# Kernel tuning notes

Hardware: AMD Instinct MI355X
Metric: run time of the kernel (lower is better)

Reference implementation:

```python
import jax, jax.numpy as jnp
import numpy as np

B, T = 8, 1024          # batch, sequence length
C = 512                 # hidden_channels
FC = 2048               # filter_channels
H = 8                   # n_heads
L = 6                   # n_layers
KS = 3                  # ffn kernel_size
WS = 4                  # relative-attention window_size
KC = C // H             # per-head channels
SCALE = float(KC) ** 0.5
EPS = 1e-5


def setup_inputs():
    key = jax.random.key(0)
    ks = jax.random.split(key, 10)
    def nrm(k, shape, s=0.02):
        return jax.random.normal(k, shape, dtype=jnp.float32) * s
    return {
        "x": jax.random.normal(ks[0], (B, C, T), dtype=jnp.float32),
        "x_mask": jnp.ones((B, 1, T), dtype=jnp.float32),
        "qw": nrm(ks[1], (L, C, C)), "qb": jnp.zeros((L, C), jnp.float32),
        "kw": nrm(ks[2], (L, C, C)), "kb": jnp.zeros((L, C), jnp.float32),
        "vw": nrm(ks[3], (L, C, C)), "vb": jnp.zeros((L, C), jnp.float32),
        "ow": nrm(ks[4], (L, C, C)), "ob": jnp.zeros((L, C), jnp.float32),
        "erk": nrm(ks[5], (L, 2 * WS + 1, KC), KC ** -0.5),
        "erv": nrm(ks[6], (L, 2 * WS + 1, KC), KC ** -0.5),
        "ln1_g": jnp.ones((L, C), jnp.float32), "ln1_b": jnp.zeros((L, C), jnp.float32),
        "fw1": nrm(ks[7], (L, FC, C, KS)), "fb1": jnp.zeros((L, FC), jnp.float32),
        "fw2": nrm(ks[8], (L, C, FC, KS)), "fb2": jnp.zeros((L, C), jnp.float32),
        "ln2_g": jnp.ones((L, C), jnp.float32), "ln2_b": jnp.zeros((L, C), jnp.float32),
    }


def _get_rel_emb(emb, length, ws):
    # emb: [2*ws+1, d] (heads_share=True) -> [2*length-1, d]
    pad = max(length - (ws + 1), 0)
    start = max(ws + 1 - length, 0)
    padded = jnp.pad(emb, ((pad, pad), (0, 0)))
    return padded[start:start + 2 * length - 1]


def _rel_to_abs(x):
    # [b,h,l,2l-1] -> [b,h,l,l]  (VITS pad/reshape trick)
    b, h, l, _ = x.shape
    x = jnp.pad(x, ((0, 0), (0, 0), (0, 0), (0, 1))).reshape(b, h, l * 2 * l)
    x = jnp.pad(x, ((0, 0), (0, 0), (0, l - 1))).reshape(b, h, l + 1, 2 * l - 1)
    return x[:, :, :l, l - 1:]


def _abs_to_rel(x):
    # [b,h,l,l] -> [b,h,l,2l-1]
    b, h, l, _ = x.shape
    x = jnp.pad(x, ((0, 0), (0, 0), (0, 0), (0, l - 1))).reshape(b, h, l * (2 * l - 1))
    x = jnp.pad(x, ((0, 0), (0, 0), (l, 0))).reshape(b, h, l, 2 * l)
    return x[:, :, :, 1:]


def _proj(x, w, b):
    # 1x1 conv1d: x [b,c,t], w [o,c]
    return jnp.einsum('bct,oc->bot', x, w) + b[None, :, None]


def _layer_norm_c(x, g, b):
    # LayerNorm over channel dim of [b,c,t]
    m = jnp.mean(x, axis=1, keepdims=True)
    v = jnp.mean(jnp.square(x - m), axis=1, keepdims=True)
    return (x - m) * jax.lax.rsqrt(v + EPS) * g[None, :, None] + b[None, :, None]


def _attention(x, qw, qb, kw, kb, vw, vb, ow, ob, erk, erv, mask_bias):
    b, _, t = x.shape
    def split_heads(y):
        return y.reshape(b, H, KC, t).transpose(0, 1, 3, 2)  # [b,h,t,kc]
    q = split_heads(_proj(x, qw, qb)) / SCALE
    k = split_heads(_proj(x, kw, kb))
    v = split_heads(_proj(x, vw, vb))
    scores = jnp.einsum('bhtd,bhsd->bhts', q, k)
    rel_k = _get_rel_emb(erk, t, WS)                       # [2t-1, kc]
    scores = scores + _rel_to_abs(jnp.einsum('bhld,md->bhlm', q, rel_k))
    scores = scores + mask_bias
    p = jax.nn.softmax(scores, axis=-1)
    out = jnp.einsum('bhts,bhsd->bhtd', p, v)
    rel_v = _get_rel_emb(erv, t, WS)
    out = out + jnp.einsum('bhlm,md->bhld', _abs_to_rel(p), rel_v)
    out = out.transpose(0, 1, 3, 2).reshape(b, C, t)       # merge heads -> [b,c,t]
    return _proj(out, ow, ob)


def _conv1d(x, w, b):
    pad = ((KS - 1) // 2, KS // 2)  # _same_padding
    y = jax.lax.conv_general_dilated(x, w, (1,), [pad],
                                     dimension_numbers=('NCH', 'OIH', 'NCH'))
    return y + b[None, :, None]


def _ffn(x, x_mask, w1, b1, w2, b2):
    h = jax.nn.relu(_conv1d(x * x_mask, w1, b1))  # activation=None -> relu
    return _conv1d(h * x_mask, w2, b2) * x_mask


def reference(x, x_mask, qw, qb, kw, kb, vw, vb, ow, ob, erk, erv,
              ln1_g, ln1_b, fw1, fb1, fw2, fb2, ln2_g, ln2_b):
    attn_mask = x_mask[:, :, None, :] * x_mask[:, :, :, None]  # [b,1,t,t]
    mask_bias = jnp.where(attn_mask != 0, 0.0, -1e4).astype(x.dtype)
    x = x * x_mask
    for i in range(L):
        y = _attention(x, qw[i], qb[i], kw[i], kb[i], vw[i], vb[i],
                       ow[i], ob[i], erk[i], erv[i], mask_bias)
        x = _layer_norm_c(x + y, ln1_g[i], ln1_b[i])
        y = _ffn(x, x_mask, fw1[i], fb1[i], fw2[i], fb2[i])
        x = _layer_norm_c(x + y, ln2_g[i], ln2_b[i])
    return x * x_mask
```

## Files before the change

### kernel.cpp

```cpp
#include <hip/hip_runtime.h>
#include <hip/hip_bf16.h>
#include <math.h>

#define T_LEN 1024
#define NB    8
#define CCH   512
#define FCH   2048
#define NH    8
#define HD    64
#define NL    6
#define TP    1032
#define LOG2E 1.44269504f

typedef short bf16x8 __attribute__((ext_vector_type(8)));
typedef float f32x4  __attribute__((ext_vector_type(4)));

typedef __attribute__((address_space(1))) const void gvoid_t;
typedef __attribute__((address_space(3))) void lvoid_t;

static __device__ __forceinline__ float b2f(short s) {
    union { unsigned u; float f; } cv; cv.u = ((unsigned)(unsigned short)s) << 16; return cv.f;
}
static __device__ __forceinline__ short f2b(float f) {
    union { __hip_bfloat16 h; short s; } cv; cv.h = __float2bfloat16(f); return cv.s;
}
static __device__ __forceinline__ float exp2_hw(float x) {
    float r; asm("v_exp_f32 %0, %1" : "=v"(r) : "v"(x)); return r;
}

__global__ __launch_bounds__(512)
void conv1_256(const short* __restrict__ Xb, const short* __restrict__ Wb,
               const float* __restrict__ Bias, short* __restrict__ outB)
{
    __shared__ short abuf[2][256 * 64];
    __shared__ short bbuf[2][256 * 64];

    const int tid  = threadIdx.x;
    const int wave = tid >> 6, lane = tid & 63;
    const int l15  = lane & 15, l16 = lane >> 4;
    const int wm   = wave >> 2, wn = wave & 3;
    const int srow = lane >> 3;
    const int xsw  = ((lane & 7) ^ (srow & 7)) << 3;

    const int t0 = blockIdx.x * 256;
    const int o0 = blockIdx.y * 256;
    const int b  = blockIdx.z;

    constexpr int NK = 24;
    const size_t arow0 = (size_t)b * TP + t0;

    auto stageA = [&](int kcg, short* dst) {
        const int tap = kcg >> 3;
        const int c0  = (kcg & 7) << 6;
        const short* base = Xb + (arow0 + tap) * CCH + c0 + xsw;
        #pragma unroll
        for (int i = 0; i < 4; ++i) {
            const int j = wave + 8 * i;
            __builtin_amdgcn_global_load_lds((gvoid_t*)(base + (size_t)(j * 8 + srow) * CCH),
                                             (lvoid_t*)(dst + j * 512), 16, 0, 0);
        }
    };
    auto stageB = [&](int kcg, short* dst) {
        const int tap = kcg >> 3;
        const int c0  = (kcg & 7) << 6;
        const short* base = Wb + ((size_t)tap * FCH + o0) * CCH + c0 + xsw;
        #pragma unroll
        for (int i = 0; i < 4; ++i) {
            const int j = wave + 8 * i;
            __builtin_amdgcn_global_load_lds((gvoid_t*)(base + (size_t)(j * 8 + srow) * CCH),
                                             (lvoid_t*)(dst + j * 512), 16, 0, 0);
        }
    };

    f32x4 acc[8][4];
    #pragma unroll
    for (int i = 0; i < 8; ++i)
        #pragma unroll
        for (int j = 0; j < 4; ++j) acc[i][j] = (f32x4){0.f, 0.f, 0.f, 0.f};

    stageA(0, abuf[0]);
    stageB(0, bbuf[0]);

    for (int kc = 0; kc < NK; ++kc) {
        const int cur = kc & 1, nxt = cur ^ 1;
        const int kn  = (kc + 1 < NK) ? (kc + 1) : kc;

        __builtin_amdgcn_s_barrier();
        stageA(kn, abuf[nxt]);
        asm volatile("s_waitcnt vmcnt(4)" ::: "memory");
        __builtin_amdgcn_s_barrier();

        #pragma unroll
        for (int ks = 0; ks < 2; ++ks) {
            if (ks == 1) stageB(kn, bbuf[nxt]);
            bf16x8 af[8], bfr[4];
            #pragma unroll
            for (int fm = 0; fm < 8; ++fm) {
                const int ra = wm * 128 + fm * 16 + l15;
                af[fm] = *(const bf16x8*)&abuf[cur][ra * 64 + (((ks * 4 + l16) ^ (ra & 7)) << 3)];
            }
            #pragma unroll
            for (int fn = 0; fn < 4; ++fn) {
                const int rb = wn * 64 + fn * 16 + l15;
                bfr[fn] = *(const bf16x8*)&bbuf[cur][rb * 64 + (((ks * 4 + l16) ^ (rb & 7)) << 3)];
            }
            __builtin_amdgcn_s_setprio(1);
            #pragma unroll
            for (int fm = 0; fm < 8; ++fm)
                #pragma unroll
                for (int fn = 0; fn < 4; ++fn)
                    acc[fm][fn] = __builtin_amdgcn_mfma_f32_16x16x32_bf16(
                        af[fm], bfr[fn], acc[fm][fn], 0, 0, 0);
            __builtin_amdgcn_s_setprio(0);
        }
    }

    float bias_v[4];
    #pragma unroll
    for (int fn = 0; fn < 4; ++fn)
        bias_v[fn] = Bias[o0 + wn * 64 + fn * 16 + l15];

    #pragma unroll
    for (int fm = 0; fm < 8; ++fm) {
        #pragma unroll
        for (int r = 0; r < 4; ++r) {
            const int t_loc = wm * 128 + fm * 16 + l16 * 4 + r;
            const size_t orow = (size_t)b * TP + t0 + t_loc + 1;
            #pragma unroll
            for (int fn = 0; fn < 4; ++fn) {
                const int o = o0 + wn * 64 + fn * 16 + l15;
                outB[orow * FCH + o] = f2b(fmaxf(acc[fm][fn][r] + bias_v[fn], 0.f));
            }
        }
    }

    if (t0 == 0)
        for (int cc = tid; cc < 256; cc += 512)
            outB[((size_t)b * TP) * FCH + o0 + cc] = 0;
    if (t0 == T_LEN - 256)
        for (int idx = tid; idx < 7 * 256; idx += 512) {
            const int rr = idx >> 8, cc = idx & 255;
            outB[((size_t)b * TP + 1025 + rr) * FCH + o0 + cc] = 0;
        }
}

template<int KSZ, bool RELU, int OMODE, bool VTOUT>
__global__ __launch_bounds__(256)
void mfma_gemm(const short* __restrict__ Xb, const short* __restrict__ Wb,
               const float* __restrict__ Bias,
               short* __restrict__ outB1, short* __restrict__ outB2,
               short* __restrict__ VTout,
               int Cin, int O, int ksplit)
{
    constexpr int XR = (KSZ == 3) ? 136 : 128;
    __shared__ short shmem[(XR + 128) * 64];
    short* xl = shmem;
    short* wl = shmem + XR * 64;

    const int tid  = threadIdx.x;
    const int wave = tid >> 6, lane = tid & 63;
    const int l15  = lane & 15, l16 = lane >> 4;
    const int wm   = wave >> 1, wn = wave & 1;

    const int t0 = blockIdx.x * 128;
    const int o0 = blockIdx.y * 128;
    const int zz = blockIdx.z;
    const int b     = zz / ksplit;
    const int split = zz - b * ksplit;
    const int kcin  = Cin / ksplit;
    const int cbeg  = split * kcin;

    const size_t xrowbase = (KSZ == 3) ? ((size_t)b * TP + t0) : (size_t)t0;

    const int srow = lane >> 3;
    const int xsw  = ((lane & 7) ^ (srow & 7)) << 3;

    f32x4 acc[4][4];
    #pragma unroll
    for (int i = 0; i < 4; ++i)
        #pragma unroll
        for (int j = 0; j < 4; ++j) acc[i][j] = (f32x4){0.f, 0.f, 0.f, 0.f};

    for (int cb = 0; cb < kcin; cb += 64) {
        const int c0 = cbeg + cb;
        __syncthreads();
        for (int j = wave; j < XR / 8; j += 4) {
            const short* src = Xb + (xrowbase + (size_t)(j * 8 + srow)) * Cin + c0 + xsw;
            __builtin_amdgcn_global_load_lds((gvoid_t*)src, (lvoid_t*)&xl[j * 512], 16, 0, 0);
        }
        #pragma unroll
        for (int kk = 0; kk < KSZ; ++kk) {
            if (kk > 0) __syncthreads();
            for (int j = wave; j < 16; j += 4) {
                const short* src = Wb + ((size_t)kk * O + o0 + j * 8 + srow) * Cin + c0 + xsw;
                __builtin_amdgcn_global_load_lds((gvoid_t*)src, (lvoid_t*)&wl[j * 512], 16, 0, 0);
            }
            __syncthreads();
            #pragma unroll
            for (int ks = 0; ks < 2; ++ks) {
                bf16x8 af[4], bfr[4];
                #pragma unroll
                for (int f = 0; f < 4; ++f) {
                    const int ra = wm * 64 + f * 16 + l15 + (KSZ == 3 ? kk : 0);
                    af[f] = *(const bf16x8*)&xl[ra * 64 + (((ks * 4 + l16) ^ (ra & 7)) << 3)];
                    const int rb = wn * 64 + f * 16 + l15;
                    bfr[f] = *(const bf16x8*)&wl[rb * 64 + (((ks * 4 + l16) ^ (rb & 7)) << 3)];
                }
                #pragma unroll
                for (int fm = 0; fm < 4; ++fm)
                    #pragma unroll
                    for (int fn = 0; fn < 4; ++fn)
                        acc[fm][fn] = __builtin_amdgcn_mfma_f32_16x16x32_bf16(
                            af[fm], bfr[fn], acc[fm][fn], 0, 0, 0);
            }
        }
    }

    float bias_v[4];
    #pragma unroll
    for (int fn = 0; fn < 4; ++fn)
        bias_v[fn] = (OMODE != 2 || split == 0) ? Bias[o0 + wn * 64 + fn * 16 + l15] : 0.f;

    const bool vtblk = VTOUT && (o0 >= 1024);

    if (vtblk) {
        __syncthreads();
        short* tb = shmem;
        #pragma unroll
        for (int fm = 0; fm < 4; ++fm)
            #pragma unroll
            for (int r = 0; r < 4; ++r) {
                const int t_loc = wm * 64 + fm * 16 + l16 * 4 + r;
                #pragma unroll
                for (int fn = 0; fn < 4; ++fn) {
                    const int ol = wn * 64 + fn * 16 + l15;
                    tb[ol * 128 + (((t_loc >> 3) ^ (ol & 7)) << 3) + (t_loc & 7)]
                        = f2b(acc[fm][fn][r] + bias_v[fn]);
                }
            }
        __syncthreads();
        const int bq  = t0 >> 10, tin = t0 & 1023;
        const int vcb = o0 - 1024;
        #pragma unroll
        for (int p = 0; p < 8; ++p) {
            const int drow  = (tid >> 4) + p * 16;
            const int chunk = tid & 15;
            bf16x8 v = *(const bf16x8*)&tb[drow * 128 + ((chunk ^ (drow & 7)) << 3)];
            const int vc = vcb + drow;
            *(bf16x8*)&VTout[((size_t)(bq * NH + (vc >> 6)) * HD + (vc & 63)) * T_LEN
                             + tin + chunk * 8] = v;
        }
    } else {
        #pragma unroll
        for (int fm = 0; fm < 4; ++fm) {
            #pragma unroll
            for (int r = 0; r < 4; ++r) {
                const int t_loc = wm * 64 + fm * 16 + l16 * 4 + r;
                const size_t orow = (KSZ == 3) ? ((size_t)b * T_LEN + t0 + t_loc)
                                               : (size_t)(t0 + t_loc);
                #pragma unroll
                for (int fn = 0; fn < 4; ++fn) {
                    const int o = o0 + wn * 64 + fn * 16 + l15;
                    float v = acc[fm][fn][r] + bias_v[fn];
                    if (RELU) v = fmaxf(v, 0.f);
                    const size_t idx = orow * (size_t)O + o;
                    if (OMODE == 2) {
                        if (split == 0) outB1[idx] = f2b(v);
                        else            outB2[idx] = f2b(v);
                    } else {
                        outB1[idx] = f2b(v);
                    }
                }
            }
        }
    }
}

__global__ __launch_bounds__(512)
void attn_mfma(const short* __restrict__ QKV, const short* __restrict__ VT,
               const float* __restrict__ erk, const float* __restrict__ erv,
               short* __restrict__ Yat)
{
    const int n = blockIdx.x;
    const int c = n & 7, g = n >> 3;
    const int bh = c * 8 + (g & 7);
    const int qt = g >> 3;
    const int b = bh >> 3, h = bh & 7;
    const int tq0 = qt * 128;
    const int hq = h * HD;
    const size_t bt0 = (size_t)b * T_LEN;

    __shared__ short ql[128 * 64];
    __shared__ short pl0[128 * 64];
    __shared__ short kl[2][64 * 64];
    __shared__ short vl[2][64 * 64];
    __shared__ float qerkl[128][12];
    __shared__ float ervl[9][64];

    const int tid  = threadIdx.x;
    const int wave = tid >> 6, lane = tid & 63;
    const int l15  = lane & 15, l16 = lane >> 4;
    const int srow = lane >> 3;
    const int xsw  = ((lane & 7) ^ (srow & 7)) << 3;

    const short* vbase = VT + (size_t)bh * HD * T_LEN;

    for (int j = wave; j < 16; j += 8) {
        const short* src = QKV + (bt0 + tq0 + j * 8 + srow) * 1536 + hq + xsw;
        __builtin_amdgcn_global_load_lds((gvoid_t*)src, (lvoid_t*)&ql[j * 512], 16, 0, 0);
    }
    {
        const short* ksrc = QKV + (bt0 + wave * 8 + srow) * 1536 + 512 + hq + xsw;
        __builtin_amdgcn_global_load_lds((gvoid_t*)ksrc, (lvoid_t*)&kl[0][wave * 512], 16, 0, 0);
        const short* vsrc = vbase + (size_t)(wave * 8 + srow) * T_LEN + xsw;
        __builtin_amdgcn_global_load_lds((gvoid_t*)vsrc, (lvoid_t*)&vl[0][wave * 512], 16, 0, 0);
    }
    for (int i = tid; i < 9 * 64; i += 512) ervl[i >> 6][i & 63] = erv[i];
    __syncthreads();

    bf16x8 af[2];
    #pragma unroll
    for (int ks = 0; ks < 2; ++ks) {
        const int r0 = wave * 16 + l15;
        af[ks] = *(const bf16x8*)&ql[r0 * 64 + (((ks * 4 + l16) ^ (r0 & 7)) << 3)];
    }

    for (int idx = tid; idx < 128 * 9; idx += 512) {
        const int r = idx / 9, o = idx - r * 9;
        float s = 0.f;
        for (int d = 0; d < 64; ++d) {
            float qv = b2f(ql[r * 64 + (((d >> 3) ^ (r & 7)) << 3) + (d & 7)]);
            s += qv * erk[o * 64 + d];
        }
        qerkl[r][o] = s;
    }

    float lsum[4] = {0.f, 0.f, 0.f, 0.f};
    f32x4 acco[4];
    #pragma unroll
    for (int fn = 0; fn < 4; ++fn) acco[fn] = (f32x4){0.f, 0.f, 0.f, 0.f};
    bf16x8 vf[2][4];

    const int ra = wave * 16 + l15;

    for (int it = 0; it < 16; ++it) {
        const int cur = it & 1;
        const int s0  = it * 64;
        __syncthreads();

        if (it < 15) {
            const short* ksrc = QKV + (bt0 + s0 + 64 + wave * 8 + srow) * 1536 + 512 + hq + xsw;
            __builtin_amdgcn_global_load_lds((gvoid_t*)ksrc, (lvoid_t*)&kl[cur ^ 1][wave * 512], 16, 0, 0);
            const short* vsrc = vbase + (size_t)(wave * 8 + srow) * T_LEN + s0 + 64 + xsw;
            __builtin_amdgcn_global_load_lds((gvoid_t*)vsrc, (lvoid_t*)&vl[cur ^ 1][wave * 512], 16, 0, 0);
        }

        f32x4 sc[4];
        #pragma unroll
        for (int fn = 0; fn < 4; ++fn) sc[fn] = (f32x4){0.f, 0.f, 0.f, 0.f};
        __builtin_amdgcn_s_setprio(1);
        #pragma unroll
        for (int ks = 0; ks < 2; ++ks)
            #pragma unroll
            for (int fn = 0; fn < 4; ++fn) {
                const int rb = fn * 16 + l15;
                bf16x8 bf = *(const bf16x8*)&kl[cur][rb * 64 + (((ks * 4 + l16) ^ (rb & 7)) << 3)];
                sc[fn] = __builtin_amdgcn_mfma_f32_16x16x32_bf16(af[ks], bf, sc[fn], 0, 0, 0);
            }
        __builtin_amdgcn_s_setprio(0);

        if (it > 0) {
            short* plp = cur ? pl0 : ql;
            __builtin_amdgcn_s_setprio(1);
            #pragma unroll
            for (int ks = 0; ks < 2; ++ks) {
                bf16x8 paf = *(const bf16x8*)&plp[ra * 64 + (((ks * 4 + l16) ^ (ra & 7)) << 3)];
                #pragma unroll
                for (int fn = 0; fn < 4; ++fn)
                    acco[fn] = __builtin_amdgcn_mfma_f32_16x16x32_bf16(paf, vf[ks][fn], acco[fn], 0, 0, 0);
            }
            __builtin_amdgcn_s_setprio(0);
            const int s0p = s0 - 64;
            if ((s0p >= tq0 - 64) && (s0p <= tq0 + 128)) {
                #pragma unroll
                for (int r = 0; r < 4; ++r) {
                    const int q_loc = wave * 16 + l16 * 4 + r;
                    const int qg = tq0 + q_loc;
                    #pragma unroll
                    for (int o = 0; o < 9; ++o) {
                        const int jj = qg + o - 4 - s0p;
                        if (jj >= 0 && jj < 64) {
                            const float p = b2f(plp[q_loc * 64
                                + (((jj >> 3) ^ (q_loc & 7)) << 3) + (jj & 7)]);
                            #pragma unroll
                            for (int fn = 0; fn < 4; ++fn)
                                acco[fn][r] += p * ervl[o][fn * 16 + l15];
                        }
                    }
                }
            }
        }

        #pragma unroll
        for (int ks = 0; ks < 2; ++ks)
            #pragma unroll
            for (int fn = 0; fn < 4; ++fn) {
                const int rb = fn * 16 + l15;
                vf[ks][fn] = *(const bf16x8*)&vl[cur][rb * 64 + (((ks * 4 + l16) ^ (rb & 7)) << 3)];
            }

        if ((s0 >= tq0 - 64) && (s0 <= tq0 + 128)) {
            #pragma unroll
            for (int fn = 0; fn < 4; ++fn)
                #pragma unroll
                for (int r = 0; r < 4; ++r) {
                    const int q_loc = wave * 16 + l16 * 4 + r;
                    const int off = (s0 + fn * 16 + l15) - (tq0 + q_loc);
                    if (off >= -4 && off <= 4)
                        sc[fn][r] += qerkl[q_loc][off + 4];
                }
        }
        #pragma unroll
        for (int fn = 0; fn < 4; ++fn)
            #pragma unroll
            for (int r = 0; r < 4; ++r) {
                const float p = exp2_hw(sc[fn][r]);
                sc[fn][r] = p;
                lsum[r] += p;
            }

        {
            short* plw = cur ? ql : pl0;
            #pragma unroll
            for (int fn = 0; fn < 4; ++fn)
                #pragma unroll
                for (int r = 0; r < 4; ++r) {
                    const int q_loc = wave * 16 + l16 * 4 + r;
                    const int s_loc = fn * 16 + l15;
                    plw[q_loc * 64 + (((s_loc >> 3) ^ (q_loc & 7)) << 3) + (s_loc & 7)]
                        = f2b(sc[fn][r]);
                }
        }
    }

    __syncthreads();
    {
        short* plp = ql;
        #pragma unroll
        for (int ks = 0; ks < 2; ++ks) {
            bf16x8 paf = *(const bf16x8*)&plp[ra * 64 + (((ks * 4 + l16) ^ (ra & 7)) << 3)];
            #pragma unroll
            for (int fn = 0; fn < 4; ++fn)
                acco[fn] = __builtin_amdgcn_mfma_f32_16x16x32_bf16(paf, vf[ks][fn], acco[fn], 0, 0, 0);
        }
        const int s0p = 960;
        if ((s0p >= tq0 - 64) && (s0p <= tq0 + 128)) {
            #pragma unroll
            for (int r = 0; r < 4; ++r) {
                const int q_loc = wave * 16 + l16 * 4 + r;
                const int qg = tq0 + q_loc;
                #pragma unroll
                for (int o = 0; o < 9; ++o) {
                    const int jj = qg + o - 4 - s0p;
                    if (jj >= 0 && jj < 64) {
                        const float p = b2f(plp[q_loc * 64
                            + (((jj >> 3) ^ (q_loc & 7)) << 3) + (jj & 7)]);
                        #pragma unroll
                        for (int fn = 0; fn < 4; ++fn)
                            acco[fn][r] += p * ervl[o][fn * 16 + l15];
                    }
                }
            }
        }
    }

    #pragma unroll
    for (int r = 0; r < 4; ++r) {
        float l = lsum[r];
        l += __shfl_xor(l, 1);
        l += __shfl_xor(l, 2);
        l += __shfl_xor(l, 4);
        l += __shfl_xor(l, 8);
        const float inv = 1.f / l;
        const int q_loc = wave * 16 + l16 * 4 + r;
        const size_t row = (bt0 + tq0 + q_loc) * CCH + hq;
        #pragma unroll
        for (int fn = 0; fn < 4; ++fn)
            Yat[row + fn * 16 + l15] = f2b(acco[fn][r] * inv);
    }
}

__global__ __launch_bounds__(256)
void ln_kernel(const short* __restrict__ X, const short* __restrict__ Y1b,
               const short* __restrict__ Y2b, const float* __restrict__ g,
               const float* __restrict__ bb, short* __restrict__ outB,
               int xpad, int opad)
{
    const int wave = threadIdx.x >> 6, lane = threadIdx.x & 63;
    const int row  = blockIdx.x * 4 + wave;
    const int c = lane * 8;
    const size_t frow = (size_t)row * CCH + c;
    const size_t prow = ((size_t)(row >> 10) * TP + (row & 1023) + 1) * CCH + c;

    float v[8];
    {
        bf16x8 s = *(const bf16x8*)&X[xpad ? prow : frow];
        #pragma unroll
        for (int j = 0; j < 8; ++j) v[j] = b2f(s[j]);
    }
    {
        bf16x8 s = *(const bf16x8*)&Y1b[frow];
        #pragma unroll
        for (int j = 0; j < 8; ++j) v[j] += b2f(s[j]);
    }
    if (Y2b) {
        bf16x8 s = *(const bf16x8*)&Y2b[frow];
        #pragma unroll
        for (int j = 0; j < 8; ++j) v[j] += b2f(s[j]);
    }
    float s1 = 0.f, s2 = 0.f;
    #pragma unroll
    for (int j = 0; j < 8; ++j) { s1 += v[j]; s2 += v[j] * v[j]; }
    #pragma unroll
    for (int off = 1; off < 64; off <<= 1) {
        s1 += __shfl_xor(s1, off);
        s2 += __shfl_xor(s2, off);
    }
    const float mu = s1 * (1.f / CCH);
    const float rs = rsqrtf(s2 * (1.f / CCH) - mu * mu + 1e-5f);

    const float4 g0 = *(const float4*)&g[c], g1 = *(const float4*)&g[c + 4];
    const float4 b0 = *(const float4*)&bb[c], b1 = *(const float4*)&bb[c + 4];
    float o[8];
    o[0] = (v[0] - mu) * rs * g0.x + b0.x;
    o[1] = (v[1] - mu) * rs * g0.y + b0.y;
    o[2] = (v[2] - mu) * rs * g0.z + b0.z;
    o[3] = (v[3] - mu) * rs * g0.w + b0.w;
    o[4] = (v[4] - mu) * rs * g1.x + b1.x;
    o[5] = (v[5] - mu) * rs * g1.y + b1.y;
    o[6] = (v[6] - mu) * rs * g1.z + b1.z;
    o[7] = (v[7] - mu) * rs * g1.w + b1.w;

    bf16x8 pk;
    #pragma unroll
    for (int j = 0; j < 8; ++j) pk[j] = f2b(o[j]);
    *(bf16x8*)&outB[opad ? prow : frow] = pk;
}

__global__ __launch_bounds__(256)
void transpose_in(const float* __restrict__ x, short* __restrict__ curb)
{
    __shared__ float tl[32][33];
    const int tx = threadIdx.x & 31, ty = threadIdx.x >> 5;
    const int t0 = blockIdx.x * 32, c0 = blockIdx.y * 32, b = blockIdx.z;
    #pragma unroll
    for (int i = 0; i < 4; ++i)
        tl[ty + i * 8][tx] = x[((size_t)b * CCH + c0 + ty + i * 8) * T_LEN + t0 + tx];
    __syncthreads();
    #pragma unroll
    for (int i = 0; i < 4; ++i) {
        const size_t orow = (size_t)b * T_LEN + t0 + ty + i * 8;
        curb[orow * CCH + c0 + tx] = f2b(tl[tx][ty + i * 8]);
    }
}

__global__ __launch_bounds__(256)
void transpose_out(const short* __restrict__ curb, float* __restrict__ out)
{
    __shared__ float tl[32][33];
    const int tx = threadIdx.x & 31, ty = threadIdx.x >> 5;
    const int t0 = blockIdx.x * 32, c0 = blockIdx.y * 32, b = blockIdx.z;
    #pragma unroll
    for (int i = 0; i < 4; ++i)
        tl[ty + i * 8][tx] = b2f(curb[((size_t)b * T_LEN + t0 + ty + i * 8) * CCH + c0 + tx]);
    __syncthreads();
    #pragma unroll
    for (int i = 0; i < 4; ++i)
        out[((size_t)b * CCH + c0 + ty + i * 8) * T_LEN + t0 + tx] = tl[tx][ty + i * 8];
}

__global__ __launch_bounds__(256)
void wconv_all(const float* __restrict__ qw, const float* __restrict__ kw,
               const float* __restrict__ vw, const float* __restrict__ ow,
               const float* __restrict__ qb, const float* __restrict__ kb,
               const float* __restrict__ vb,
               const float* __restrict__ fw1, const float* __restrict__ fw2,
               short* __restrict__ wqkv, short* __restrict__ wo,
               float* __restrict__ biasq,
               short* __restrict__ wf1o, short* __restrict__ wf2o)
{
    const int sec = blockIdx.y;
    const int idx = blockIdx.x * 256 + threadIdx.x;
    if (sec == 0) {
        const int sel = idx >> 18, r = idx & 262143;
        float v;
        if (sel == 0)      v = qw[r] * (0.125f * LOG2E);
        else if (sel == 1) v = kw[r];
        else if (sel == 2) v = vw[r];
        else               v = ow[r];
        if (sel < 3) wqkv[sel * 262144 + r] = f2b(v);
        else         wo[r] = f2b(v);
        if (idx < 1536) {
            float bv;
            if (idx < 512)       bv = qb[idx] * (0.125f * LOG2E);
            else if (idx < 1024) bv = kb[idx - 512];
            else                 bv = vb[idx - 1024];
            biasq[idx] = bv;
        }
    } else {
        const float* fw = (sec == 1) ? fw1 : fw2;
        short* out      = (sec == 1) ? wf1o : wf2o;
        const int OC = FCH * CCH;
        const float w0 = fw[3 * idx + 0];
        const float w1 = fw[3 * idx + 1];
        const float w2 = fw[3 * idx + 2];
        out[idx]          = f2b(w0);
        out[OC + idx]     = f2b(w1);
        out[2 * OC + idx] = f2b(w2);
    }
}

__global__ __launch_bounds__(256)
void zero_pads(short* __restrict__ p, int C)
{
    const int idx = blockIdx.x * 256 + threadIdx.x;
    const int r = idx / C, c = idx - r * C;
    if (r >= 64) return;
    const int batch = r >> 3, pr = r & 7;
    const size_t row = (size_t)batch * TP + (pr ? 1024 + pr : 0);
    p[row * C + c] = 0;
}

extern "C" void kernel_launch(void* const* d_in, const int* in_sizes, int n_in,
                              void* d_out, int out_size, void* d_ws, size_t ws_size,
                              hipStream_t stream)
{
    (void)in_sizes; (void)n_in; (void)out_size; (void)ws_size;

    const float* x    = (const float*)d_in[0];
    const float* qw   = (const float*)d_in[2];
    const float* qb   = (const float*)d_in[3];
    const float* kw   = (const float*)d_in[4];
    const float* kb   = (const float*)d_in[5];
    const float* vw   = (const float*)d_in[6];
    const float* vb   = (const float*)d_in[7];
    const float* ow   = (const float*)d_in[8];
    const float* obp  = (const float*)d_in[9];
    const float* erk  = (const float*)d_in[10];
    const float* erv  = (const float*)d_in[11];
    const float* ln1g = (const float*)d_in[12];
    const float* ln1b = (const float*)d_in[13];
    const float* fw1  = (const float*)d_in[14];
    const float* fb1  = (const float*)d_in[15];
    const float* fw2  = (const float*)d_in[16];
    const float* fb2  = (const float*)d_in[17];
    const float* ln2g = (const float*)d_in[18];
    const float* ln2b = (const float*)d_in[19];

    char* w = (char*)d_ws;
    size_t off = 0;
    auto alloc = [&](size_t bytes) { char* p = w + off; off += (bytes + 255) & ~(size_t)255; return p; };

    short* wqkv_b = (short*)alloc(1536 * 512 * 2);
    short* wo_b   = (short*)alloc(512 * 512 * 2);
    float* biasq  = (float*)alloc(1536 * 4);
    short* wf1_b  = (short*)alloc((size_t)3 * FCH * CCH * 2);
    short* wf2_b  = (short*)alloc((size_t)3 * CCH * FCH * 2);
    short* curb   = (short*)alloc((size_t)NB * T_LEN * CCH * 2);
    char*  uni    = alloc((size_t)NB * TP * FCH * 2);
    short* qkvf   = (short*)uni;
    short* at     = (short*)(uni + (size_t)NB * T_LEN * 1536 * 2);
    short* hbb    = (short*)uni;
    short* vty    = (short*)alloc((size_t)NB * NH * HD * T_LEN * 2);
    short* yb1b   = (short*)alloc((size_t)NB * T_LEN * CCH * 2);
    short* xAb    = (short*)alloc((size_t)NB * TP * CCH * 2);

    short* VT   = vty;
    short* y2s0 = vty;

    const dim3 blk(256);

    zero_pads<<<dim3((64 * CCH + 255) / 256), blk, 0, stream>>>(xAb, CCH);
    transpose_in<<<dim3(32, 16, NB), blk, 0, stream>>>(x, curb);

    for (int i = 0; i < NL; ++i) {
        const size_t woff = (size_t)i * CCH * CCH;
        wconv_all<<<dim3(4096, 3), blk, 0, stream>>>(
            qw + woff, kw + woff, vw + woff, ow + woff,
            qb + i * CCH, kb + i * CCH, vb + i * CCH,
            fw1 + (size_t)i * FCH * CCH * 3, fw2 + (size_t)i * CCH * FCH * 3,
            wqkv_b, wo_b, biasq, wf1_b, wf2_b);

        mfma_gemm<1, false, 0, true><<<dim3(64, 12, 1), blk, 0, stream>>>(
            curb, wqkv_b, biasq, qkvf, nullptr, VT, CCH, 1536, 1);

        attn_mfma<<<dim3(512), dim3(512), 0, stream>>>(
            qkvf, VT, erk + (size_t)i * 9 * HD, erv + (size_t)i * 9 * HD, at);

        mfma_gemm<1, false, 0, false><<<dim3(64, 4, 1), blk, 0, stream>>>(
            at, wo_b, obp + i * CCH, yb1b, nullptr, nullptr, CCH, CCH, 1);

        ln_kernel<<<dim3(2048), blk, 0, stream>>>(
            curb, yb1b, nullptr, ln1g + i * CCH, ln1b + i * CCH, xAb, 0, 1);

        conv1_256<<<dim3(4, 8, NB), dim3(512), 0, stream>>>(
            xAb, wf1_b, fb1 + i * FCH, hbb);

        mfma_gemm<3, false, 2, false><<<dim3(8, 4, NB * 2), blk, 0, stream>>>(
            hbb, wf2_b, fb2 + i * CCH, y2s0, yb1b, nullptr, FCH, CCH, 2);

        ln_kernel<<<dim3(2048), blk, 0, stream>>>(
            xAb, y2s0, yb1b, ln2g + i * CCH, ln2b + i * CCH, curb, 1, 0);
    }

    transpose_out<<<dim3(32, 16, NB), blk, 0, stream>>>(curb, (float*)d_out);
}
```

Baseline: 1.415 ms.

## Double-buffer GEMM LDS tiles and flatten conv taps into K loop

Restructures the MFMA GEMM main loop to use double-buffered LDS tiles for both X and W. The next chunk's loads are issued while the current chunk is computed, with partial vmcnt waits and raw barriers in place of full syncs. The conv taps are flattened into the K iteration, so each tap reloads a 128-row X tile instead of reusing the 136-row halo tile. MFMA sections are also wrapped in setprio. The aim is to hide global-to-LDS latency, at the cost of more LDS, more X loads, and delicate ordering between waitcnt and barriers.

```diff
diff --git a/kernel.cpp b/kernel.cpp
--- a/kernel.cpp
+++ b/kernel.cpp
@@ -152,28 +152,50 @@
                short* __restrict__ VTout,
                int Cin, int O, int ksplit)
 {
-    constexpr int XR = (KSZ == 3) ? 136 : 128;
-    __shared__ short shmem[(XR + 128) * 64];
-    short* xl = shmem;
-    short* wl = shmem + XR * 64;
+    __shared__ short abuf[2][128 * 64];
+    __shared__ short bbuf[2][128 * 64];
 
     const int tid  = threadIdx.x;
     const int wave = tid >> 6, lane = tid & 63;
     const int l15  = lane & 15, l16 = lane >> 4;
     const int wm   = wave >> 1, wn = wave & 1;
+    const int srow = lane >> 3;
+    const int xsw  = ((lane & 7) ^ (srow & 7)) << 3;
 
     const int t0 = blockIdx.x * 128;
     const int o0 = blockIdx.y * 128;
     const int zz = blockIdx.z;
     const int b     = zz / ksplit;
     const int split = zz - b * ksplit;
-    const int kcin  = Cin / ksplit;
-    const int cbeg  = split * kcin;
+
+    const int cpt = Cin >> 6;
+    const int NK  = (cpt * KSZ) / ksplit;
+    const int kbase = split * NK;
 
     const size_t xrowbase = (KSZ == 3) ? ((size_t)b * TP + t0) : (size_t)t0;
 
-    const int srow = lane >> 3;
-    const int xsw  = ((lane & 7) ^ (srow & 7)) << 3;
+    auto stageA = [&](int kcg, short* dst) {
+        const int tap = (KSZ == 3) ? (kcg / cpt) : 0;
+        const int c0  = (kcg - tap * cpt) << 6;
+        const short* base = Xb + (xrowbase + tap) * Cin + c0 + xsw;
+        #pragma unroll
+        for (int i = 0; i < 4; ++i) {
+            const int j = wave + 4 * i;
+            __builtin_amdgcn_global_load_lds((gvoid_t*)(base + (size_t)(j * 8 + srow) * Cin),
+                                             (lvoid_t*)(dst + j * 512), 16, 0, 0);
+        }
+    };
+    auto stageB = [&](int kcg, short* dst) {
+        const int tap = (KSZ == 3) ? (kcg / cpt) : 0;
+        const int c0  = (kcg - tap * cpt) << 6;
+        const short* base = Wb + ((size_t)tap * O + o0) * Cin + c0 + xsw;
+        #pragma unroll
+        for (int i = 0; i < 4; ++i) {
+            const int j = wave + 4 * i;
+            __builtin_amdgcn_global_load_lds((gvoid_t*)(base + (size_t)(j * 8 + srow) * Cin),
+                                             (lvoid_t*)(dst + j * 512), 16, 0, 0);
+        }
+    };
 
     f32x4 acc[4][4];
     #pragma unroll
@@ -181,38 +203,37 @@
         #pragma unroll
         for (int j = 0; j < 4; ++j) acc[i][j] = (f32x4){0.f, 0.f, 0.f, 0.f};
 
-    for (int cb = 0; cb < kcin; cb += 64) {
-        const int c0 = cbeg + cb;
-        __syncthreads();
-        for (int j = wave; j < XR / 8; j += 4) {
-            const short* src = Xb + (xrowbase + (size_t)(j * 8 + srow)) * Cin + c0 + xsw;
-            __builtin_amdgcn_global_load_lds((gvoid_t*)src, (lvoid_t*)&xl[j * 512], 16, 0, 0);
-        }
-        #pragma unroll
-        for (int kk = 0; kk < KSZ; ++kk) {
-            if (kk > 0) __syncthreads();
-            for (int j = wave; j < 16; j += 4) {
-                const short* src = Wb + ((size_t)kk * O + o0 + j * 8 + srow) * Cin + c0 + xsw;
-                __builtin_amdgcn_global_load_lds((gvoid_t*)src, (lvoid_t*)&wl[j * 512], 16, 0, 0);
-            }
-            __syncthreads();
-            #pragma unroll
-            for (int ks = 0; ks < 2; ++ks) {
-                bf16x8 af[4], bfr[4];
-                #pragma unroll
-                for (int f = 0; f < 4; ++f) {
-                    const int ra = wm * 64 + f * 16 + l15 + (KSZ == 3 ? kk : 0);
-                    af[f] = *(const bf16x8*)&xl[ra * 64 + (((ks * 4 + l16) ^ (ra & 7)) << 3)];
-                    const int rb = wn * 64 + f * 16 + l15;
-                    bfr[f] = *(const bf16x8*)&wl[rb * 64 + (((ks * 4 + l16) ^ (rb & 7)) << 3)];
-                }
-                #pragma unroll
-                for (int fm = 0; fm < 4; ++fm)
-                    #pragma unroll
-                    for (int fn = 0; fn < 4; ++fn)
-                        acc[fm][fn] = __builtin_amdgcn_mfma_f32_16x16x32_bf16(
-                            af[fm], bfr[fn], acc[fm][fn], 0, 0, 0);
-            }
+    stageA(kbase, abuf[0]);
+    stageB(kbase, bbuf[0]);
+
+    for (int kc = 0; kc < NK; ++kc) {
+        const int cur = kc & 1, nxt = cur ^ 1;
+        const int kn  = kbase + ((kc + 1 < NK) ? (kc + 1) : kc);
+
+        __builtin_amdgcn_s_barrier();
+        stageA(kn, abuf[nxt]);
+        asm volatile("s_waitcnt vmcnt(4)" ::: "memory");
+        __builtin_amdgcn_s_barrier();
+
+        #pragma unroll
+        for (int ks = 0; ks < 2; ++ks) {
+            if (ks == 1) stageB(kn, bbuf[nxt]);
+            bf16x8 af[4], bfr[4];
+            #pragma unroll
+            for (int f = 0; f < 4; ++f) {
+                const int ra = wm * 64 + f * 16 + l15;
+                af[f] = *(const bf16x8*)&abuf[cur][ra * 64 + (((ks * 4 + l16) ^ (ra & 7)) << 3)];
+                const int rb = wn * 64 + f * 16 + l15;
+                bfr[f] = *(const bf16x8*)&bbuf[cur][rb * 64 + (((ks * 4 + l16) ^ (rb & 7)) << 3)];
+            }
+            __builtin_amdgcn_s_setprio(1);
+            #pragma unroll
+            for (int fm = 0; fm < 4; ++fm)
+                #pragma unroll
+                for (int fn = 0; fn < 4; ++fn)
+                    acc[fm][fn] = __builtin_amdgcn_mfma_f32_16x16x32_bf16(
+                        af[fm], bfr[fn], acc[fm][fn], 0, 0, 0);
+            __builtin_amdgcn_s_setprio(0);
         }
     }
 
@@ -224,8 +245,9 @@
     const bool vtblk = VTOUT && (o0 >= 1024);
 
     if (vtblk) {
+        asm volatile("s_waitcnt vmcnt(0)" ::: "memory");
         __syncthreads();
-        short* tb = shmem;
+        short* tb = &abuf[0][0];
         #pragma unroll
         for (int fm = 0; fm < 4; ++fm)
             #pragma unroll
```

Result: slower. 1.645 ms (+16.3%).
